# Performance work log

Hardware: AMD Instinct MI355X
Metric: run time of the kernel (lower is better)

## Reference

```python
import jax, jax.numpy as jnp
import numpy as np

B, NI, LS, D, H, W, LAB = 512, 256, 64, 8, 128, 256, 10
L = LS - 1          # logsig_dim - 1 (leading term dropped)
NSTEPS = 256        # fixed Tsit5 steps over [t0, t1]

# Tsit5 Butcher tableau (Tsitouras 2011)
C2, C3, C4, C5, C6 = 0.161, 0.327, 0.9, 0.9800255409045097, 1.0
A21 = 0.161
A31, A32 = -0.008480655492356989, 0.335480655492357
A41, A42, A43 = 2.8971530571054935, -6.359448489975075, 4.3622954328695815
A51, A52, A53, A54 = 5.325864828439257, -11.748883564062828, 7.4955393428898365, -0.09249506636175525
A61, A62, A63, A64, A65 = 5.86145544294642, -12.92096931784711, 8.159367898576159, -0.071584973281401, -0.028269050394068383
B1, B2, B3, B4, B5, B6 = 0.09646076681806523, 0.01, 0.4798896504144996, 1.379008574103742, -3.290069515436081, 2.324710524099774


def setup_inputs() -> dict:
    key = jax.random.key(0)
    ks = jax.random.split(key, 8)

    def lin(k, out_d, in_d):  # eqx.nn.Linear default init: U(-1/sqrt(in), 1/sqrt(in))
        kw, kb = jax.random.split(k)
        lim = 1.0 / np.sqrt(in_d)
        Wm = jax.random.uniform(kw, (out_d, in_d), minval=-lim, maxval=lim, dtype=jnp.float32)
        bv = jax.random.uniform(kb, (out_d,), minval=-lim, maxval=lim, dtype=jnp.float32)
        return Wm, bv

    W0, b0 = lin(ks[0], W, H)        # VF MLP layer 1
    W1, b1 = lin(ks[1], W, W)        # VF MLP layer 2
    W2, b2 = lin(ks[2], H * L, W)    # VF MLP output layer
    l1w, l1b = lin(ks[3], H, D)      # linear1
    l2w, l2b = lin(ks[4], LAB, H)    # linear2

    ts = jnp.linspace(0.0, 1.0, NI + 1, dtype=jnp.float32)
    intervals = ts[1:]               # right endpoints for searchsorted lookup
    logsig = 0.1 * jax.random.normal(ks[5], (B, NI, LS), dtype=jnp.float32)
    x0 = jax.random.normal(ks[6], (B, D), dtype=jnp.float32)
    return dict(ts=ts, intervals=intervals, logsig=logsig, x0=x0,
                W0=W0, b0=b0, W1=W1, b1=b1, W2=W2, b2=b2,
                l1w=l1w, l1b=l1b, l2w=l2w, l2b=l2b)


def _forward(ts, intervals, logsig, x0, W0, b0, W1, b1, W2, b2, l1w, l1b, l2w, l2b):
    def f(t, y):  # y: [B, H] -> dy/dt: [B, H]
        idx = jnp.clip(jnp.searchsorted(intervals, t), 0, NI - 1)
        h = jax.nn.silu(y @ W0.T + b0)
        h = jax.nn.silu(h @ W1.T + b1)
        A = jnp.tanh(h @ W2.T + b2).reshape(-1, H, L)   # [B, H, L]
        g = logsig[:, idx, 1:]                           # [B, L]
        return jnp.einsum('bhl,bl->bh', A, g)

    y0 = x0 @ l1w.T + l1b                                # linear1
    dt = (ts[-1] - ts[0]) / NSTEPS

    @jax.checkpoint
    def step(carry, _):
        t, y = carry
        k1 = f(t, y)
        k2 = f(t + C2 * dt, y + dt * (A21 * k1))
        k3 = f(t + C3 * dt, y + dt * (A31 * k1 + A32 * k2))
        k4 = f(t + C4 * dt, y + dt * (A41 * k1 + A42 * k2 + A43 * k3))
        k5 = f(t + C5 * dt, y + dt * (A51 * k1 + A52 * k2 + A53 * k3 + A54 * k4))
        k6 = f(t + C6 * dt, y + dt * (A61 * k1 + A62 * k2 + A63 * k3 + A64 * k4 + A65 * k5))
        y_new = y + dt * (B1 * k1 + B2 * k2 + B3 * k3 + B4 * k4 + B5 * k5 + B6 * k6)
        return (t + dt, y_new), None

    (_, yf), _ = jax.lax.scan(step, (ts[0], y0), None, length=NSTEPS)
    return jax.nn.softmax(yf @ l2w.T + l2b, axis=-1)     # classification head


def reference(ts, intervals, logsig, x0, W0, b0, W1, b1, W2, b2, l1w, l1b, l2w, l2b):
    return _forward(ts, intervals, logsig, x0, W0, b0, W1, b1, W2, b2, l1w, l1b, l2w, l2b)
```

## Files before the change

### kernel.cpp

```cpp
#include <hip/hip_runtime.h>

typedef __attribute__((ext_vector_type(8))) short short8;
typedef __attribute__((ext_vector_type(4))) float f32x4;
typedef unsigned long long ull;

#define DT (1.0f/256.0f)
#define NSTEPS 256

__device__ __forceinline__ short f2bf(float f) {
    unsigned u = __float_as_uint(f);
    u = (u + 0x7fffu + ((u >> 16) & 1u)) >> 16;
    return (short)u;
}
__device__ __forceinline__ unsigned cvtpk(float a, float b) {
    unsigned r;
    asm("v_cvt_pk_bf16_f32 %0, %1, %2" : "=v"(r) : "v"(a), "v"(b));
    return r;
}
__device__ __forceinline__ float fast_silu(float x) {
    float e = __expf(-x);
    return x * __builtin_amdgcn_rcpf(1.f + e);
}
__device__ __forceinline__ float fast_tanh(float x) {
    float e = __expf(2.f * x);
    return 1.f - 2.f * __builtin_amdgcn_rcpf(e + 1.f);
}

__device__ __forceinline__ void st_agent_f(float* p, float v) {
    __hip_atomic_store(p, v, __ATOMIC_RELAXED, __HIP_MEMORY_SCOPE_AGENT);
}
__device__ __forceinline__ void st_agent_u32(unsigned* p, unsigned v) {
    __hip_atomic_store(p, v, __ATOMIC_RELAXED, __HIP_MEMORY_SCOPE_AGENT);
}
__device__ __forceinline__ ull ld_agent_u64(const void* p) {
    return __hip_atomic_load((const ull*)p, __ATOMIC_RELAXED, __HIP_MEMORY_SCOPE_AGENT);
}

__global__ void perm_w0(const float* __restrict__ W0, short* __restrict__ W0p) {
    int i = blockIdx.x * 256 + threadIdx.x;
    int j = i & 7, l = (i >> 3) & 63, kc = (i >> 9) & 3, ot = i >> 11;
    int row = ot * 16 + (l & 15);
    int col = kc * 32 + ((l >> 4) << 3) + j;
    W0p[i] = f2bf(W0[row * 128 + col]);
}
__global__ void perm_w1(const float* __restrict__ W1, short* __restrict__ W1p) {
    int i = blockIdx.x * 256 + threadIdx.x;
    int j = i & 7, l = (i >> 3) & 63, kc = (i >> 9) & 7, ot = i >> 12;
    int row = ot * 16 + (l & 15);
    int col = kc * 32 + ((l >> 4) << 3) + j;
    W1p[i] = f2bf(W1[row * 256 + col]);
}
__global__ void perm_w2(const float* __restrict__ W2, short* __restrict__ W2p) {
    int i = blockIdx.x * 256 + threadIdx.x;
    int j = i & 7, ln = (i >> 3) & 63, kc = (i >> 9) & 7;
    int q4 = (i >> 12) & 15, ht = i >> 16;
    int m = ln & 15;
    int hl = m & 3, lvin = m >> 2;
    int lv = q4 * 4 + lvin;
    if (lv >= 63) { W2p[i] = 0; return; }
    int row = (ht * 4 + hl) * 63 + lv;
    int col = kc * 32 + ((ln >> 4) << 3) + j;
    W2p[i] = f2bf(W2[row * 256 + col]);
}

__global__ void y0_kernel(const float* __restrict__ x0, const float* __restrict__ l1w,
                          const float* __restrict__ l1b, float* __restrict__ y0f,
                          unsigned short* __restrict__ ybf) {
    int i = blockIdx.x * 256 + threadIdx.x;
    int b = i >> 7, h = i & 127;
    float s = l1b[h];
    #pragma unroll
    for (int d = 0; d < 8; ++d) s += x0[b * 8 + d] * l1w[h * 8 + d];
    y0f[i] = s;
    ybf[i] = (unsigned short)f2bf(s);
}

struct Smem {
    alignas(16) short ysb[64 * 136];
    alignas(16) short h1b[64 * 272];
    alignas(16) short h2b[64 * 272];
    float gsh[64 * 65];
    float b2sh[4 * 64];
    float b0sh[256];
    float b1sh[256];
    float kred[8][4][4][17];
};

__constant__ const float cA2[1] = {0.161f};
__constant__ const float cA3[2] = {-0.008480655492356989f, 0.335480655492357f};
__constant__ const float cA4[3] = {2.8971530571054935f, -6.359448489975075f, 4.3622954328695815f};
__constant__ const float cA5[4] = {5.325864828439257f, -11.748883564062828f, 7.4955393428898365f, -0.09249506636175525f};
__constant__ const float cA6[5] = {5.86145544294642f, -12.92096931784711f, 8.159367898576159f, -0.071584973281401f, -0.028269050394068383f};

template<int STAGE>
__device__ __forceinline__ void do_stage(
    Smem& sm, int s, int gsi, int bg, int ht, int tid,
    unsigned short* __restrict__ ybf,
    float* __restrict__ yfinal,
    const short* __restrict__ W0p, const short* __restrict__ W1p, const short* __restrict__ W2p,
    const float* __restrict__ logsig,
    unsigned* __restrict__ barctr,
    float (&yreg)[2], float (&kr)[2][5])
{
    const int w    = tid >> 6;
    const int lane = tid & 63;
    const int q    = lane >> 4;
    const int rr   = lane & 15;
    const unsigned short* ycur = ybf + (gsi & 1) * 65536;
    unsigned short*       ynxt = ybf + ((gsi + 1) & 1) * 65536;

    short8 af0[2][4];
    #pragma unroll
    for (int oi = 0; oi < 2; ++oi)
        #pragma unroll
        for (int kc = 0; kc < 4; ++kc)
            af0[oi][kc] = *reinterpret_cast<const short8*>(W0p + ((w * 2 + oi) * 4 + kc) * 512 + lane * 8);

    if constexpr (STAGE == 2) {
        const int b = tid >> 3, l0 = (tid & 7) * 8;
        const float* gp = logsig + (bg * 64 + b) * 16384 + s * 64 + 1;
        #pragma unroll
        for (int ii = 0; ii < 8; ++ii) {
            int l = l0 + ii;
            sm.gsh[b * 65 + l] = (l < 63) ? gp[l] : 0.f;
        }
    }

    if (gsi > 0 && tid == 0) {
        const unsigned target = 32u * (unsigned)gsi;
        while (__hip_atomic_load(&barctr[bg * 16], __ATOMIC_RELAXED, __HIP_MEMORY_SCOPE_AGENT) < target) { }
    }
    __syncthreads();

    {
        const int b = tid >> 3, h0 = (tid & 7) * 16;
        const ull* src = (const ull*)(ycur + (bg * 64 + b) * 128 + h0);
        ull v0 = ld_agent_u64(src + 0);
        ull v1 = ld_agent_u64(src + 1);
        ull v2 = ld_agent_u64(src + 2);
        ull v3 = ld_agent_u64(src + 3);
        ull* dst = (ull*)&sm.ysb[b * 136 + h0];
        dst[0] = v0; dst[1] = v1; dst[2] = v2; dst[3] = v3;
    }
    __syncthreads();

    {
        f32x4 acc[2][4];
        #pragma unroll
        for (int oi = 0; oi < 2; ++oi)
            #pragma unroll
            for (int bq = 0; bq < 4; ++bq) acc[oi][bq] = (f32x4){0.f, 0.f, 0.f, 0.f};
        #pragma unroll
        for (int kc = 0; kc < 4; ++kc) {
            short8 bfr[4];
            #pragma unroll
            for (int bq = 0; bq < 4; ++bq)
                bfr[bq] = *reinterpret_cast<const short8*>(&sm.ysb[(bq * 16 + rr) * 136 + kc * 32 + q * 8]);
            #pragma unroll
            for (int oi = 0; oi < 2; ++oi)
                #pragma unroll
                for (int bq = 0; bq < 4; ++bq)
                    acc[oi][bq] = __builtin_amdgcn_mfma_f32_16x16x32_bf16(af0[oi][kc], bfr[bq], acc[oi][bq], 0, 0, 0);
        }
        #pragma unroll
        for (int oi = 0; oi < 2; ++oi) {
            const int ho = (w * 2 + oi) * 16 + q * 4;
            #pragma unroll
            for (int bq = 0; bq < 4; ++bq) {
                float vv[4];
                #pragma unroll
                for (int j = 0; j < 4; ++j)
                    vv[j] = fast_silu(acc[oi][bq][j] + sm.b0sh[ho + j]);
                ull pk = (ull)cvtpk(vv[0], vv[1]) | ((ull)cvtpk(vv[2], vv[3]) << 32);
                *reinterpret_cast<ull*>(&sm.h1b[(bq * 16 + rr) * 272 + ho]) = pk;
            }
        }
    }
    __syncthreads();

    {
        short8 af[2][8];
        #pragma unroll
        for (int oi = 0; oi < 2; ++oi)
            #pragma unroll
            for (int kc = 0; kc < 8; ++kc)
                af[oi][kc] = *reinterpret_cast<const short8*>(W1p + ((w * 2 + oi) * 8 + kc) * 512 + lane * 8);
        f32x4 acc[2][4];
        #pragma unroll
        for (int oi = 0; oi < 2; ++oi)
            #pragma unroll
            for (int bq = 0; bq < 4; ++bq) acc[oi][bq] = (f32x4){0.f, 0.f, 0.f, 0.f};
        #pragma unroll
        for (int kc = 0; kc < 8; ++kc) {
            short8 bfr[4];
            #pragma unroll
            for (int bq = 0; bq < 4; ++bq)
                bfr[bq] = *reinterpret_cast<const short8*>(&sm.h1b[(bq * 16 + rr) * 272 + kc * 32 + q * 8]);
            #pragma unroll
            for (int oi = 0; oi < 2; ++oi)
                #pragma unroll
                for (int bq = 0; bq < 4; ++bq)
                    acc[oi][bq] = __builtin_amdgcn_mfma_f32_16x16x32_bf16(af[oi][kc], bfr[bq], acc[oi][bq], 0, 0, 0);
        }
        #pragma unroll
        for (int oi = 0; oi < 2; ++oi) {
            const int ho = (w * 2 + oi) * 16 + q * 4;
            #pragma unroll
            for (int bq = 0; bq < 4; ++bq) {
                float vv[4];
                #pragma unroll
                for (int j = 0; j < 4; ++j)
                    vv[j] = fast_silu(acc[oi][bq][j] + sm.b1sh[ho + j]);
                ull pk = (ull)cvtpk(vv[0], vv[1]) | ((ull)cvtpk(vv[2], vv[3]) << 32);
                *reinterpret_cast<ull*>(&sm.h2b[(bq * 16 + rr) * 272 + ho]) = pk;
            }
        }
    }
    __syncthreads();

    {
        short8 af[2][8];
        #pragma unroll
        for (int t2 = 0; t2 < 2; ++t2)
            #pragma unroll
            for (int kc = 0; kc < 8; ++kc)
                af[t2][kc] = *reinterpret_cast<const short8*>(W2p + (size_t)(ht * 16 + w * 2 + t2) * 4096 + kc * 512 + lane * 8);
        f32x4 acc[2][4];
        #pragma unroll
        for (int t2 = 0; t2 < 2; ++t2)
            #pragma unroll
            for (int bq = 0; bq < 4; ++bq) acc[t2][bq] = (f32x4){0.f, 0.f, 0.f, 0.f};
        #pragma unroll
        for (int kc = 0; kc < 8; ++kc) {
            short8 bfr[4];
            #pragma unroll
            for (int bq = 0; bq < 4; ++bq)
                bfr[bq] = *reinterpret_cast<const short8*>(&sm.h2b[(bq * 16 + rr) * 272 + kc * 32 + q * 8]);
            #pragma unroll
            for (int t2 = 0; t2 < 2; ++t2)
                #pragma unroll
                for (int bq = 0; bq < 4; ++bq)
                    acc[t2][bq] = __builtin_amdgcn_mfma_f32_16x16x32_bf16(af[t2][kc], bfr[bq], acc[t2][bq], 0, 0, 0);
        }
        float kacc[4][4];
        #pragma unroll
        for (int bq = 0; bq < 4; ++bq)
            #pragma unroll
            for (int j = 0; j < 4; ++j) kacc[bq][j] = 0.f;
        #pragma unroll
        for (int t2 = 0; t2 < 2; ++t2) {
            const int lv = (w * 2 + t2) * 4 + q;
            #pragma unroll
            for (int bq = 0; bq < 4; ++bq) {
                float gv = sm.gsh[(bq * 16 + rr) * 65 + lv];
                #pragma unroll
                for (int j = 0; j < 4; ++j) {
                    float x = acc[t2][bq][j] + sm.b2sh[j * 64 + lv];
                    kacc[bq][j] += fast_tanh(x) * gv;
                }
            }
        }
        #pragma unroll
        for (int bq = 0; bq < 4; ++bq)
            #pragma unroll
            for (int j = 0; j < 4; ++j) {
                float v = kacc[bq][j];
                v += __shfl_xor(v, 16);
                v += __shfl_xor(v, 32);
                kacc[bq][j] = v;
            }
        if (q == 0) {
            #pragma unroll
            for (int bq = 0; bq < 4; ++bq)
                #pragma unroll
                for (int j = 0; j < 4; ++j)
                    sm.kred[w][bq][j][rr] = kacc[bq][j];
        }
    }
    __syncthreads();

    if (tid < 128) {
        const int b = tid >> 1, hs = tid & 1;
        float s0 = 0.f, s1 = 0.f;
        #pragma unroll
        for (int ww = 0; ww < 8; ++ww) {
            s0 += sm.kred[ww][b >> 4][hs * 2 + 0][b & 15];
            s1 += sm.kred[ww][b >> 4][hs * 2 + 1][b & 15];
        }
        float nv0, nv1;
        if constexpr (STAGE == 1) {
            kr[0][0] = s0; kr[1][0] = s1;
            nv0 = yreg[0] + DT * (cA2[0] * s0);
            nv1 = yreg[1] + DT * (cA2[0] * s1);
        } else if constexpr (STAGE == 2) {
            kr[0][1] = s0; kr[1][1] = s1;
            nv0 = yreg[0] + DT * (cA3[0] * kr[0][0] + cA3[1] * s0);
            nv1 = yreg[1] + DT * (cA3[0] * kr[1][0] + cA3[1] * s1);
        } else if constexpr (STAGE == 3) {
            kr[0][2] = s0; kr[1][2] = s1;
            nv0 = yreg[0] + DT * (cA4[0] * kr[0][0] + cA4[1] * kr[0][1] + cA4[2] * s0);
            nv1 = yreg[1] + DT * (cA4[0] * kr[1][0] + cA4[1] * kr[1][1] + cA4[2] * s1);
        } else if constexpr (STAGE == 4) {
            kr[0][3] = s0; kr[1][3] = s1;
            nv0 = yreg[0] + DT * (cA5[0] * kr[0][0] + cA5[1] * kr[0][1] + cA5[2] * kr[0][2] + cA5[3] * s0);
            nv1 = yreg[1] + DT * (cA5[0] * kr[1][0] + cA5[1] * kr[1][1] + cA5[2] * kr[1][2] + cA5[3] * s1);
        } else if constexpr (STAGE == 5) {
            kr[0][4] = s0; kr[1][4] = s1;
            nv0 = yreg[0] + DT * (cA6[0] * kr[0][0] + cA6[1] * kr[0][1] + cA6[2] * kr[0][2] + cA6[3] * kr[0][3] + cA6[4] * s0);
            nv1 = yreg[1] + DT * (cA6[0] * kr[1][0] + cA6[1] * kr[1][1] + cA6[2] * kr[1][2] + cA6[3] * kr[1][3] + cA6[4] * s1);
        } else {
            nv0 = yreg[0] + DT * (0.09646076681806523f * kr[0][0] + 0.01f * kr[0][1]
                 + 0.4798896504144996f * kr[0][2] + 1.379008574103742f * kr[0][3]
                 + (-3.290069515436081f) * kr[0][4] + 2.324710524099774f * s0);
            nv1 = yreg[1] + DT * (0.09646076681806523f * kr[1][0] + 0.01f * kr[1][1]
                 + 0.4798896504144996f * kr[1][2] + 1.379008574103742f * kr[1][3]
                 + (-3.290069515436081f) * kr[1][4] + 2.324710524099774f * s1);
            yreg[0] = nv0; yreg[1] = nv1;
        }
        const int gi = (bg * 64 + b) * 128 + ht * 4 + hs * 2;
        st_agent_u32(reinterpret_cast<unsigned*>(ynxt + gi), cvtpk(nv0, nv1));
        if constexpr (STAGE == 6) {
            if (s == NSTEPS - 1) {
                st_agent_f(&yfinal[gi], nv0);
                st_agent_f(&yfinal[gi + 1], nv1);
            }
        }
    }

    __syncthreads();
    if (tid == 0)
        __hip_atomic_fetch_add(&barctr[bg * 16], 1u, __ATOMIC_RELAXED, __HIP_MEMORY_SCOPE_AGENT);
}

__global__ __launch_bounds__(512, 2) void rde_persistent(
    float* y0f, unsigned short* ybf, float* yfinal, unsigned* barctr,
    const short* W0p, const short* W1p, const short* W2p,
    const float* b0, const float* b1, const float* b2,
    const float* logsig)
{
    __shared__ Smem sm;
    const int tid = threadIdx.x;
    const int bg  = blockIdx.x >> 5;
    const int ht  = blockIdx.x & 31;
    if (tid < 256) {
        sm.b0sh[tid] = b0[tid];
        int hl = tid >> 6, lv = tid & 63;
        sm.b2sh[tid] = (lv < 63) ? b2[(ht * 4 + hl) * 63 + lv] : 0.f;
    } else {
        sm.b1sh[tid - 256] = b1[tid - 256];
    }
    {
        const int b = tid >> 3, l0 = (tid & 7) * 8;
        const float* gp = logsig + (bg * 64 + b) * 16384 + 1;
        #pragma unroll
        for (int ii = 0; ii < 8; ++ii) {
            int l = l0 + ii;
            sm.gsh[b * 65 + l] = (l < 63) ? gp[l] : 0.f;
        }
    }
    float yreg[2] = {0.f, 0.f};
    float kr[2][5] = {{0.f,0.f,0.f,0.f,0.f},{0.f,0.f,0.f,0.f,0.f}};
    if (tid < 128) {
        const int b = tid >> 1, hs = tid & 1;
        const int gi = (bg * 64 + b) * 128 + ht * 4 + hs * 2;
        yreg[0] = y0f[gi];
        yreg[1] = y0f[gi + 1];
    }
    #pragma unroll 1
    for (int s = 0; s < NSTEPS; ++s) {
        const int g6 = s * 6;
        do_stage<1>(sm, s, g6 + 0, bg, ht, tid, ybf, yfinal, W0p, W1p, W2p, logsig, barctr, yreg, kr);
        do_stage<2>(sm, s, g6 + 1, bg, ht, tid, ybf, yfinal, W0p, W1p, W2p, logsig, barctr, yreg, kr);
        do_stage<3>(sm, s, g6 + 2, bg, ht, tid, ybf, yfinal, W0p, W1p, W2p, logsig, barctr, yreg, kr);
        do_stage<4>(sm, s, g6 + 3, bg, ht, tid, ybf, yfinal, W0p, W1p, W2p, logsig, barctr, yreg, kr);
        do_stage<5>(sm, s, g6 + 4, bg, ht, tid, ybf, yfinal, W0p, W1p, W2p, logsig, barctr, yreg, kr);
        do_stage<6>(sm, s, g6 + 5, bg, ht, tid, ybf, yfinal, W0p, W1p, W2p, logsig, barctr, yreg, kr);
    }
}

__global__ void out_kernel(const float* __restrict__ yf, const float* __restrict__ l2w,
                           const float* __restrict__ l2b, float* __restrict__ out) {
    int b = blockIdx.x, t = threadIdx.x;
    float ya = yf[b * 128 + t], yb = yf[b * 128 + 64 + t];
    __shared__ float lg[10];
    for (int c = 0; c < 10; ++c) {
        float p = ya * l2w[c * 128 + t] + yb * l2w[c * 128 + 64 + t];
        for (int off = 32; off > 0; off >>= 1) p += __shfl_down(p, off);
        if (t == 0) lg[c] = p + l2b[c];
    }
    __syncthreads();
    if (t == 0) {
        float m = lg[0];
        for (int c = 1; c < 10; ++c) m = fmaxf(m, lg[c]);
        float s = 0.f, e[10];
        for (int c = 0; c < 10; ++c) { e[c] = expf(lg[c] - m); s += e[c]; }
        for (int c = 0; c < 10; ++c) out[b * 10 + c] = e[c] / s;
    }
}

extern "C" void kernel_launch(void* const* d_in, const int* in_sizes, int n_in,
                              void* d_out, int out_size, void* d_ws, size_t ws_size,
                              hipStream_t stream) {
    const float* logsig = (const float*)d_in[2];
    const float* x0  = (const float*)d_in[3];
    const float* W0  = (const float*)d_in[4];
    const float* b0  = (const float*)d_in[5];
    const float* W1  = (const float*)d_in[6];
    const float* b1  = (const float*)d_in[7];
    const float* W2  = (const float*)d_in[8];
    const float* b2  = (const float*)d_in[9];
    const float* l1w = (const float*)d_in[10];
    const float* l1b = (const float*)d_in[11];
    const float* l2w = (const float*)d_in[12];
    const float* l2b = (const float*)d_in[13];
    float* out = (float*)d_out;

    char* ws = (char*)d_ws;
    float*          y0f    = (float*)(ws);
    unsigned short* ybf    = (unsigned short*)(ws + 262144);
    float*          yfinal = (float*)(ws + 524288);
    short*          W0p    = (short*)(ws + 786432);
    short*          W1p    = (short*)(ws + 851968);
    short*          W2p    = (short*)(ws + 983040);
    unsigned*       barctr = (unsigned*)(ws + 5177344);

    hipMemsetAsync(barctr, 0, 32 * 16 * sizeof(unsigned), stream);
    perm_w0<<<128, 256, 0, stream>>>(W0, W0p);
    perm_w1<<<256, 256, 0, stream>>>(W1, W1p);
    perm_w2<<<8192, 256, 0, stream>>>(W2, W2p);
    y0_kernel<<<256, 256, 0, stream>>>(x0, l1w, l1b, y0f, ybf);

    void* args[] = {&y0f, &ybf, &yfinal, &barctr, &W0p, &W1p, &W2p, &b0, &b1, &b2, &logsig};
    hipLaunchCooperativeKernel((const void*)rde_persistent, dim3(256), dim3(512), args, 0, stream);

    out_kernel<<<512, 64, 0, stream>>>(yfinal, l2w, l2b, out);
}
```

Before: 15.82 ms.

## Split each block's batch group into two halves and interleave their RK stages

Each persistent block now owns two independent 32-row batch groups instead of one 64-row group, and alternates RK stages between them. While one half waits on its cross-block spin barrier, the other half computes, so barrier latency and global y exchange are meant to be hidden. The number of batch groups and barrier counters doubles. The trade-off is that each stage reloads the W0/W1/W2 fragments twice as often for half-size MFMA tiles, and there are twice as many __syncthreads and barrier waits per step.

```diff
diff --git a/kernel.cpp b/kernel.cpp
--- a/kernel.cpp
+++ b/kernel.cpp
@@ -76,14 +76,15 @@
 }
 
 struct Smem {
-    alignas(16) short ysb[64 * 136];
-    alignas(16) short h1b[64 * 272];
-    alignas(16) short h2b[64 * 272];
-    float gsh[64 * 65];
+    alignas(16) short ysb[32 * 136];
+    alignas(16) short h1b[32 * 272];
+    alignas(16) short h2b[32 * 272];
+    float gshA[32 * 65];
+    float gshB[32 * 65];
     float b2sh[4 * 64];
     float b0sh[256];
     float b1sh[256];
-    float kred[8][4][4][17];
+    float kred[8][2][4][17];
 };
 
 __constant__ const float cA2[1] = {0.161f};
@@ -94,7 +95,7 @@
 
 template<int STAGE>
 __device__ __forceinline__ void do_stage(
-    Smem& sm, int s, int gsi, int bg, int ht, int tid,
+    Smem& sm, float* __restrict__ gsh, int s, int gsi, int bg, int ht, int tid,
     unsigned short* __restrict__ ybf,
     float* __restrict__ yfinal,
     const short* __restrict__ W0p, const short* __restrict__ W1p, const short* __restrict__ W2p,
@@ -117,12 +118,12 @@
             af0[oi][kc] = *reinterpret_cast<const short8*>(W0p + ((w * 2 + oi) * 4 + kc) * 512 + lane * 8);
 
     if constexpr (STAGE == 2) {
-        const int b = tid >> 3, l0 = (tid & 7) * 8;
-        const float* gp = logsig + (bg * 64 + b) * 16384 + s * 64 + 1;
-        #pragma unroll
-        for (int ii = 0; ii < 8; ++ii) {
+        const int b = tid >> 4, l0 = (tid & 15) * 4;
+        const float* gp = logsig + (bg * 32 + b) * 16384 + s * 64 + 1;
+        #pragma unroll
+        for (int ii = 0; ii < 4; ++ii) {
             int l = l0 + ii;
-            sm.gsh[b * 65 + l] = (l < 63) ? gp[l] : 0.f;
+            gsh[b * 65 + l] = (l < 63) ? gp[l] : 0.f;
         }
     }
 
@@ -133,40 +134,38 @@
     __syncthreads();
 
     {
-        const int b = tid >> 3, h0 = (tid & 7) * 16;
-        const ull* src = (const ull*)(ycur + (bg * 64 + b) * 128 + h0);
+        const int b = tid >> 4, h0 = (tid & 15) * 8;
+        const ull* src = (const ull*)(ycur + (bg * 32 + b) * 128 + h0);
         ull v0 = ld_agent_u64(src + 0);
         ull v1 = ld_agent_u64(src + 1);
-        ull v2 = ld_agent_u64(src + 2);
-        ull v3 = ld_agent_u64(src + 3);
         ull* dst = (ull*)&sm.ysb[b * 136 + h0];
-        dst[0] = v0; dst[1] = v1; dst[2] = v2; dst[3] = v3;
+        dst[0] = v0; dst[1] = v1;
     }
     __syncthreads();
 
     {
-        f32x4 acc[2][4];
+        f32x4 acc[2][2];
         #pragma unroll
         for (int oi = 0; oi < 2; ++oi)
             #pragma unroll
-            for (int bq = 0; bq < 4; ++bq) acc[oi][bq] = (f32x4){0.f, 0.f, 0.f, 0.f};
+            for (int bq = 0; bq < 2; ++bq) acc[oi][bq] = (f32x4){0.f, 0.f, 0.f, 0.f};
         #pragma unroll
         for (int kc = 0; kc < 4; ++kc) {
-            short8 bfr[4];
-            #pragma unroll
-            for (int bq = 0; bq < 4; ++bq)
+            short8 bfr[2];
+            #pragma unroll
+            for (int bq = 0; bq < 2; ++bq)
                 bfr[bq] = *reinterpret_cast<const short8*>(&sm.ysb[(bq * 16 + rr) * 136 + kc * 32 + q * 8]);
             #pragma unroll
             for (int oi = 0; oi < 2; ++oi)
                 #pragma unroll
-                for (int bq = 0; bq < 4; ++bq)
+                for (int bq = 0; bq < 2; ++bq)
                     acc[oi][bq] = __builtin_amdgcn_mfma_f32_16x16x32_bf16(af0[oi][kc], bfr[bq], acc[oi][bq], 0, 0, 0);
         }
         #pragma unroll
         for (int oi = 0; oi < 2; ++oi) {
             const int ho = (w * 2 + oi) * 16 + q * 4;
             #pragma unroll
-            for (int bq = 0; bq < 4; ++bq) {
+            for (int bq = 0; bq < 2; ++bq) {
                 float vv[4];
                 #pragma unroll
                 for (int j = 0; j < 4; ++j)
@@ -185,28 +184,28 @@
             #pragma unroll
             for (int kc = 0; kc < 8; ++kc)
                 af[oi][kc] = *reinterpret_cast<const short8*>(W1p + ((w * 2 + oi) * 8 + kc) * 512 + lane * 8);
-        f32x4 acc[2][4];
+        f32x4 acc[2][2];
         #pragma unroll
         for (int oi = 0; oi < 2; ++oi)
             #pragma unroll
-            for (int bq = 0; bq < 4; ++bq) acc[oi][bq] = (f32x4){0.f, 0.f, 0.f, 0.f};
+            for (int bq = 0; bq < 2; ++bq) acc[oi][bq] = (f32x4){0.f, 0.f, 0.f, 0.f};
         #pragma unroll
         for (int kc = 0; kc < 8; ++kc) {
-            short8 bfr[4];
-            #pragma unroll
-            for (int bq = 0; bq < 4; ++bq)
+            short8 bfr[2];
+            #pragma unroll
+            for (int bq = 0; bq < 2; ++bq)
                 bfr[bq] = *reinterpret_cast<const short8*>(&sm.h1b[(bq * 16 + rr) * 272 + kc * 32 + q * 8]);
             #pragma unroll
             for (int oi = 0; oi < 2; ++oi)
                 #pragma unroll
-                for (int bq = 0; bq < 4; ++bq)
+                for (int bq = 0; bq < 2; ++bq)
                     acc[oi][bq] = __builtin_amdgcn_mfma_f32_16x16x32_bf16(af[oi][kc], bfr[bq], acc[oi][bq], 0, 0, 0);
         }
         #pragma unroll
         for (int oi = 0; oi < 2; ++oi) {
             const int ho = (w * 2 + oi) * 16 + q * 4;
             #pragma unroll
-            for (int bq = 0; bq < 4; ++bq) {
+            for (int bq = 0; bq < 2; ++bq) {
                 float vv[4];
                 #pragma unroll
                 for (int j = 0; j < 4; ++j)
@@ -225,34 +224,34 @@
             #pragma unroll
             for (int kc = 0; kc < 8; ++kc)
                 af[t2][kc] = *reinterpret_cast<const short8*>(W2p + (size_t)(ht * 16 + w * 2 + t2) * 4096 + kc * 512 + lane * 8);
-        f32x4 acc[2][4];
+        f32x4 acc[2][2];
         #pragma unroll
         for (int t2 = 0; t2 < 2; ++t2)
             #pragma unroll
-            for (int bq = 0; bq < 4; ++bq) acc[t2][bq] = (f32x4){0.f, 0.f, 0.f, 0.f};
+            for (int bq = 0; bq < 2; ++bq) acc[t2][bq] = (f32x4){0.f, 0.f, 0.f, 0.f};
         #pragma unroll
         for (int kc = 0; kc < 8; ++kc) {
-            short8 bfr[4];
-            #pragma unroll
-            for (int bq = 0; bq < 4; ++bq)
+            short8 bfr[2];
+            #pragma unroll
+            for (int bq = 0; bq < 2; ++bq)
                 bfr[bq] = *reinterpret_cast<const short8*>(&sm.h2b[(bq * 16 + rr) * 272 + kc * 32 + q * 8]);
             #pragma unroll
             for (int t2 = 0; t2 < 2; ++t2)
                 #pragma unroll
-                for (int bq = 0; bq < 4; ++bq)
+                for (int bq = 0; bq < 2; ++bq)
                     acc[t2][bq] = __builtin_amdgcn_mfma_f32_16x16x32_bf16(af[t2][kc], bfr[bq], acc[t2][bq], 0, 0, 0);
         }
-        float kacc[4][4];
-        #pragma unroll
-        for (int bq = 0; bq < 4; ++bq)
+        float kacc[2][4];
+        #pragma unroll
+        for (int bq = 0; bq < 2; ++bq)
             #pragma unroll
             for (int j = 0; j < 4; ++j) kacc[bq][j] = 0.f;
         #pragma unroll
         for (int t2 = 0; t2 < 2; ++t2) {
             const int lv = (w * 2 + t2) * 4 + q;
             #pragma unroll
-            for (int bq = 0; bq < 4; ++bq) {
-                float gv = sm.gsh[(bq * 16 + rr) * 65 + lv];
+            for (int bq = 0; bq < 2; ++bq) {
+                float gv = gsh[(bq * 16 + rr) * 65 + lv];
                 #pragma unroll
                 for (int j = 0; j < 4; ++j) {
                     float x = acc[t2][bq][j] + sm.b2sh[j * 64 + lv];
@@ -261,7 +260,7 @@
             }
         }
         #pragma unroll
-        for (int bq = 0; bq < 4; ++bq)
+        for (int bq = 0; bq < 2; ++bq)
             #pragma unroll
             for (int j = 0; j < 4; ++j) {
                 float v = kacc[bq][j];
@@ -271,7 +270,7 @@
             }
         if (q == 0) {
             #pragma unroll
-            for (int bq = 0; bq < 4; ++bq)
+            for (int bq = 0; bq < 2; ++bq)
                 #pragma unroll
                 for (int j = 0; j < 4; ++j)
                     sm.kred[w][bq][j][rr] = kacc[bq][j];
@@ -279,7 +278,7 @@
     }
     __syncthreads();
 
-    if (tid < 128) {
+    if (tid < 64) {
         const int b = tid >> 1, hs = tid & 1;
         float s0 = 0.f, s1 = 0.f;
         #pragma unroll
@@ -317,7 +316,7 @@
                  + (-3.290069515436081f) * kr[1][4] + 2.324710524099774f * s1);
             yreg[0] = nv0; yreg[1] = nv1;
         }
-        const int gi = (bg * 64 + b) * 128 + ht * 4 + hs * 2;
+        const int gi = (bg * 32 + b) * 128 + ht * 4 + hs * 2;
         st_agent_u32(reinterpret_cast<unsigned*>(ynxt + gi), cvtpk(nv0, nv1));
         if constexpr (STAGE == 6) {
             if (s == NSTEPS - 1) {
@@ -340,8 +339,10 @@
 {
     __shared__ Smem sm;
     const int tid = threadIdx.x;
-    const int bg  = blockIdx.x >> 5;
+    const int pr  = blockIdx.x >> 5;
     const int ht  = blockIdx.x & 31;
+    const int bgA = pr * 2;
+    const int bgB = pr * 2 + 1;
     if (tid < 256) {
         sm.b0sh[tid] = b0[tid];
         int hl = tid >> 6, lv = tid & 63;
@@ -350,31 +351,41 @@
         sm.b1sh[tid - 256] = b1[tid - 256];
     }
     {
-        const int b = tid >> 3, l0 = (tid & 7) * 8;
-        const float* gp = logsig + (bg * 64 + b) * 16384 + 1;
-        #pragma unroll
-        for (int ii = 0; ii < 8; ++ii) {
+        const int b = tid >> 4, l0 = (tid & 15) * 4;
+        const float* gpA = logsig + (bgA * 32 + b) * 16384 + 1;
+        const float* gpB = logsig + (bgB * 32 + b) * 16384 + 1;
+        #pragma unroll
+        for (int ii = 0; ii < 4; ++ii) {
             int l = l0 + ii;
-            sm.gsh[b * 65 + l] = (l < 63) ? gp[l] : 0.f;
-        }
-    }
-    float yreg[2] = {0.f, 0.f};
-    float kr[2][5] = {{0.f,0.f,0.f,0.f,0.f},{0.f,0.f,0.f,0.f,0.f}};
-    if (tid < 128) {
+            sm.gshA[b * 65 + l] = (l < 63) ? gpA[l] : 0.f;
+            sm.gshB[b * 65 + l] = (l < 63) ? gpB[l] : 0.f;
+        }
+    }
+    float yrA[2] = {0.f, 0.f}, yrB[2] = {0.f, 0.f};
+    float krA[2][5] = {{0.f,0.f,0.f,0.f,0.f},{0.f,0.f,0.f,0.f,0.f}};
+    float krB[2][5] = {{0.f,0.f,0.f,0.f,0.f},{0.f,0.f,0.f,0.f,0.f}};
+    if (tid < 64) {
         const int b = tid >> 1, hs = tid & 1;
-        const int gi = (bg * 64 + b) * 128 + ht * 4 + hs * 2;
-        yreg[0] = y0f[gi];
-        yreg[1] = y0f[gi + 1];
+        const int giA = (bgA * 32 + b) * 128 + ht * 4 + hs * 2;
+        const int giB = (bgB * 32 + b) * 128 + ht * 4 + hs * 2;
+        yrA[0] = y0f[giA]; yrA[1] = y0f[giA + 1];
+        yrB[0] = y0f[giB]; yrB[1] = y0f[giB + 1];
     }
     #pragma unroll 1
     for (int s = 0; s < NSTEPS; ++s) {
         const int g6 = s * 6;
-        do_stage<1>(sm, s, g6 + 0, bg, ht, tid, ybf, yfinal, W0p, W1p, W2p, logsig, barctr, yreg, kr);
-        do_stage<2>(sm, s, g6 + 1, bg, ht, tid, ybf, yfinal, W0p, W1p, W2p, logsig, barctr, yreg, kr);
-        do_stage<3>(sm, s, g6 + 2, bg, ht, tid, ybf, yfinal, W0p, W1p, W2p, logsig, barctr, yreg, kr);
-        do_stage<4>(sm, s, g6 + 3, bg, ht, tid, ybf, yfinal, W0p, W1p, W2p, logsig, barctr, yreg, kr);
-        do_stage<5>(sm, s, g6 + 4, bg, ht, tid, ybf, yfinal, W0p, W1p, W2p, logsig, barctr, yreg, kr);
-        do_stage<6>(sm, s, g6 + 5, bg, ht, tid, ybf, yfinal, W0p, W1p, W2p, logsig, barctr, yreg, kr);
+        do_stage<1>(sm, sm.gshA, s, g6 + 0, bgA, ht, tid, ybf, yfinal, W0p, W1p, W2p, logsig, barctr, yrA, krA);
+        do_stage<1>(sm, sm.gshB, s, g6 + 0, bgB, ht, tid, ybf, yfinal, W0p, W1p, W2p, logsig, barctr, yrB, krB);
+        do_stage<2>(sm, sm.gshA, s, g6 + 1, bgA, ht, tid, ybf, yfinal, W0p, W1p, W2p, logsig, barctr, yrA, krA);
+        do_stage<2>(sm, sm.gshB, s, g6 + 1, bgB, ht, tid, ybf, yfinal, W0p, W1p, W2p, logsig, barctr, yrB, krB);
+        do_stage<3>(sm, sm.gshA, s, g6 + 2, bgA, ht, tid, ybf, yfinal, W0p, W1p, W2p, logsig, barctr, yrA, krA);
+        do_stage<3>(sm, sm.gshB, s, g6 + 2, bgB, ht, tid, ybf, yfinal, W0p, W1p, W2p, logsig, barctr, yrB, krB);
+        do_stage<4>(sm, sm.gshA, s, g6 + 3, bgA, ht, tid, ybf, yfinal, W0p, W1p, W2p, logsig, barctr, yrA, krA);
+        do_stage<4>(sm, sm.gshB, s, g6 + 3, bgB, ht, tid, ybf, yfinal, W0p, W1p, W2p, logsig, barctr, yrB, krB);
+        do_stage<5>(sm, sm.gshA, s, g6 + 4, bgA, ht, tid, ybf, yfinal, W0p, W1p, W2p, logsig, barctr, yrA, krA);
+        do_stage<5>(sm, sm.gshB, s, g6 + 4, bgB, ht, tid, ybf, yfinal, W0p, W1p, W2p, logsig, barctr, yrB, krB);
+        do_stage<6>(sm, sm.gshA, s, g6 + 5, bgA, ht, tid, ybf, yfinal, W0p, W1p, W2p, logsig, barctr, yrA, krA);
+        do_stage<6>(sm, sm.gshB, s, g6 + 5, bgB, ht, tid, ybf, yfinal, W0p, W1p, W2p, logsig, barctr, yrB, krB);
     }
 }
 
@@ -424,7 +435,7 @@
     short*          W2p    = (short*)(ws + 983040);
     unsigned*       barctr = (unsigned*)(ws + 5177344);
 
-    hipMemsetAsync(barctr, 0, 32 * 16 * sizeof(unsigned), stream);
+    hipMemsetAsync(barctr, 0, 16 * 16 * sizeof(unsigned), stream);
     perm_w0<<<128, 256, 0, stream>>>(W0, W0p);
     perm_w1<<<256, 256, 0, stream>>>(W1, W1p);
     perm_w2<<<8192, 256, 0, stream>>>(W2, W2p);
```

New measurement: 18.67 ms. 1.18x slower.
